# Performance work log

Hardware: AMD Instinct MI355X
Metric: run time of the kernel (lower is better)

Reference implementation:

```python
import jax, jax.numpy as jnp
import numpy as np
import math

D = 512; H = 8; L = 6; FF = 2048; S = 512; B = 32; IN = 64; OUT = 1
HD = D // H
EPS = 1e-5


def _pos_encoding(seq_len, d_model):
    position = jnp.arange(seq_len, dtype=jnp.float32)[:, None]
    div_term = jnp.exp(jnp.arange(0, d_model, 2, dtype=jnp.float32) * (-math.log(10000.0) / d_model))
    ang = position * div_term  # [S, D/2]
    pe = jnp.zeros((seq_len, d_model), dtype=jnp.float32)
    pe = pe.at[:, 0::2].set(jnp.sin(ang)).at[:, 1::2].set(jnp.cos(ang))
    return pe


def _layernorm(x, g, b):
    m = jnp.mean(x, axis=-1, keepdims=True)
    v = jnp.mean((x - m) ** 2, axis=-1, keepdims=True)
    return (x - m) * jax.lax.rsqrt(v + EPS) * g + b


def setup_inputs() -> dict:
    key = jax.random.key(0)
    ks = jax.random.split(key, 20)
    s = 0.02
    return {
        "src": jax.random.normal(ks[0], (B, S, IN), dtype=jnp.float32),
        "inp_w": jax.random.uniform(ks[1], (D, IN), minval=-0.1, maxval=0.1, dtype=jnp.float32),
        "inp_b": jnp.zeros((D,), dtype=jnp.float32),
        "in_proj_w": jax.random.normal(ks[2], (L, 3 * D, D), dtype=jnp.float32) * s,
        "in_proj_b": jnp.zeros((L, 3 * D), dtype=jnp.float32),
        "out_w": jax.random.normal(ks[3], (L, D, D), dtype=jnp.float32) * s,
        "out_b": jnp.zeros((L, D), dtype=jnp.float32),
        "ff_w1": jax.random.normal(ks[4], (L, FF, D), dtype=jnp.float32) * s,
        "ff_b1": jnp.zeros((L, FF), dtype=jnp.float32),
        "ff_w2": jax.random.normal(ks[5], (L, D, FF), dtype=jnp.float32) * s,
        "ff_b2": jnp.zeros((L, D), dtype=jnp.float32),
        "ln1_g": jnp.ones((L, D), dtype=jnp.float32),
        "ln1_b": jnp.zeros((L, D), dtype=jnp.float32),
        "ln2_g": jnp.ones((L, D), dtype=jnp.float32),
        "ln2_b": jnp.zeros((L, D), dtype=jnp.float32),
        "op_w1": jax.random.normal(ks[6], (FF, D), dtype=jnp.float32) * s,
        "op_b1": jnp.zeros((FF,), dtype=jnp.float32),
        "op_w2": jax.random.normal(ks[7], (OUT, FF), dtype=jnp.float32) * s,
        "op_b2": jnp.zeros((OUT,), dtype=jnp.float32),
    }


def reference(src, inp_w, inp_b, in_proj_w, in_proj_b, out_w, out_b,
              ff_w1, ff_b1, ff_w2, ff_b2, ln1_g, ln1_b, ln2_g, ln2_b,
              op_w1, op_b1, op_w2, op_b2):
    # input projection + sqrt(d_model) scale + positional encoding
    x = (src @ inp_w.T + inp_b) * math.sqrt(D)
    x = x + _pos_encoding(S, D)[None, :, :]
    scale = 1.0 / math.sqrt(HD)
    for i in range(L):
        # self-attention (torch nn.MultiheadAttention, eval mode, no mask)
        qkv = x @ in_proj_w[i].T + in_proj_b[i]            # [B,S,3D]
        q, k, v = jnp.split(qkv, 3, axis=-1)
        q = q.reshape(B, S, H, HD).transpose(0, 2, 1, 3)   # [B,H,S,HD]
        k = k.reshape(B, S, H, HD).transpose(0, 2, 1, 3)
        v = v.reshape(B, S, H, HD).transpose(0, 2, 1, 3)
        scores = jnp.einsum('bhqd,bhkd->bhqk', q, k) * scale
        attn = jax.nn.softmax(scores, axis=-1)             # [B,H,S,S]
        o = jnp.einsum('bhqk,bhkd->bhqd', attn, v)
        o = o.transpose(0, 2, 1, 3).reshape(B, S, D)
        o = o @ out_w[i].T + out_b[i]
        x = _layernorm(x + o, ln1_g[i], ln1_b[i])
        # feedforward
        h = jax.nn.relu(x @ ff_w1[i].T + ff_b1[i])
        ff = h @ ff_w2[i].T + ff_b2[i]
        x = _layernorm(x + ff, ln2_g[i], ln2_b[i])
    # take last timestep, output projection MLP
    last = x[:, -1, :]                                     # [B,D]
    h = jax.nn.relu(last @ op_w1.T + op_b1)
    return h @ op_w2.T + op_b2                             # [B,OUT]
```

## Files before the change

kernel.cpp:

```cpp
#include <hip/hip_runtime.h>

typedef short s16x8 __attribute__((ext_vector_type(8)));
typedef float f32x4 __attribute__((ext_vector_type(4)));
typedef float f32x16 __attribute__((ext_vector_type(16)));

__device__ short g_wbuf[18874368];
__device__ short g_srcb[1048576];
__device__ short g_inpwb[32768];
__device__ float g_pe[262144];
__device__ float g_hpart[256];

__device__ inline float b2f(short s) {
  union { unsigned int u; float f; } v;
  v.u = ((unsigned int)(unsigned short)s) << 16;
  return v.f;
}
__device__ inline short f2b(float f) {
  union { float f; unsigned int u; } v; v.f = f;
  unsigned int r = (v.u + 0x7fffu + ((v.u >> 16) & 1u)) >> 16;
  return (short)r;
}
__device__ inline s16x8 pack8(float4 a, float4 b) {
  s16x8 r;
  r[0] = f2b(a.x); r[1] = f2b(a.y); r[2] = f2b(a.z); r[3] = f2b(a.w);
  r[4] = f2b(b.x); r[5] = f2b(b.y); r[6] = f2b(b.z); r[7] = f2b(b.w);
  return r;
}

__device__ inline f32x4 mfma16(s16x8 a, s16x8 b, f32x4 c) {
  return __builtin_amdgcn_mfma_f32_16x16x32_bf16(a, b, c, 0, 0, 0);
}
__device__ inline f32x16 mfma32(s16x8 a, s16x8 b, f32x16 c) {
  return __builtin_amdgcn_mfma_f32_32x32x16_bf16(a, b, c, 0, 0, 0);
}

typedef const __attribute__((address_space(1))) void* as1cptr;
typedef __attribute__((address_space(3))) void* as3ptr;
__device__ inline void gl2lds16(const short* g, short* l) {
  __builtin_amdgcn_global_load_lds((as1cptr)g, (as3ptr)l, 16, 0, 0);
}

__global__ void __launch_bounds__(256)
cvt2_kernel(const float* __restrict__ i0, const float* __restrict__ i1) {
  const int b = blockIdx.x;
  const float* src; short* dst; int base;
  if (b < 512) { src = i0; dst = g_srcb; base = b; }
  else         { src = i1; dst = g_inpwb; base = b - 512; }
  const int idx = (base * 256 + threadIdx.x) * 8;
  float4 a = *(const float4*)(src + idx);
  float4 c = *(const float4*)(src + idx + 4);
  *(s16x8*)(dst + idx) = pack8(a, c);
}

__global__ void __launch_bounds__(256)
cvt6_kernel(const float* __restrict__ i0, const float* __restrict__ i1,
            const float* __restrict__ i2, const float* __restrict__ i3) {
  const int b = blockIdx.x;
  const float* src; short* dst; int base;
  if (b < 2304)      { src = i0; dst = g_wbuf;            base = b; }
  else if (b < 3072) { src = i1; dst = g_wbuf +  4718592; base = b - 2304; }
  else if (b < 6144) { src = i2; dst = g_wbuf +  6291456; base = b - 3072; }
  else               { src = i3; dst = g_wbuf + 12582912; base = b - 6144; }
  const int idx = (base * 256 + threadIdx.x) * 8;
  float4 a = *(const float4*)(src + idx);
  float4 c = *(const float4*)(src + idx + 4);
  *(s16x8*)(dst + idx) = pack8(a, c);
}

__global__ void __launch_bounds__(256)
pe_kernel() {
  const int s = blockIdx.x;
  const int n0 = threadIdx.x * 2;
  const float ang = (float)s * expf((float)n0 * -0.0179889460390160f);
  g_pe[s * 512 + n0]     = sinf(ang);
  g_pe[s * 512 + n0 + 1] = cosf(ang);
}

template <int EPI>
__global__ void __launch_bounds__(256, 3)
gemm_bt(const short* __restrict__ Ain, int woff, const float* __restrict__ bias,
        short* __restrict__ C, int M, int N, int K) {
  __shared__ short As[128 * 64];
  __shared__ short Bs[128 * 64];
  const int tid  = threadIdx.x;
  const int lane = tid & 63;
  const int wave = tid >> 6;
  const int wr = (wave >> 1) << 6;
  const int wc = (wave & 1) << 6;
  const int l31 = lane & 31;
  const int half = lane >> 5;
  const int bm = blockIdx.x & 127;
  const int bn = blockIdx.x >> 7;

  const short* A = (EPI == 2) ? (const short*)g_srcb : Ain;
  const short* W = (EPI == 2) ? (const short*)g_inpwb : (const short*)(g_wbuf + woff);

  int srow[4], soff[4];
#pragma unroll
  for (int i = 0; i < 4; ++i) {
    const int u = i * 256 + tid;
    srow[i] = u >> 3;
    soff[i] = ((u & 7) ^ ((u >> 3) & 7)) << 3;
  }
  const int rsw = lane & 7;
  f32x16 acc[2][2] = {};

  for (int k0 = 0; k0 < K; k0 += 64) {
#pragma unroll
    for (int i = 0; i < 4; ++i) {
      gl2lds16(A + (size_t)(bm * 128 + srow[i]) * K + k0 + soff[i],
               As + (i * 256 + tid) * 8);
      gl2lds16(W + (size_t)(bn * 128 + srow[i]) * K + k0 + soff[i],
               Bs + (i * 256 + tid) * 8);
    }
    __syncthreads();
#pragma unroll
    for (int ks = 0; ks < 4; ++ks) {
      const int rchunk = ((ks * 2 + half) ^ rsw) * 8;
      s16x8 af[2], bfr[2];
#pragma unroll
      for (int i = 0; i < 2; ++i)
        af[i] = *(const s16x8*)(As + (wr + i * 32 + l31) * 64 + rchunk);
#pragma unroll
      for (int j = 0; j < 2; ++j)
        bfr[j] = *(const s16x8*)(Bs + (wc + j * 32 + l31) * 64 + rchunk);
#pragma unroll
      for (int i = 0; i < 2; ++i)
#pragma unroll
        for (int j = 0; j < 2; ++j)
          acc[i][j] = mfma32(af[i], bfr[j], acc[i][j]);
    }
    __syncthreads();
  }

#pragma unroll
  for (int j = 0; j < 2; ++j) {
    const int col = bn * 128 + wc + j * 32 + l31;
    const float bv = bias[col];
#pragma unroll
    for (int i = 0; i < 2; ++i) {
      const int rbase = bm * 128 + wr + i * 32 + half * 4;
#pragma unroll
      for (int r = 0; r < 16; ++r) {
        const int row = rbase + (r & 3) + 8 * (r >> 2);
        float v = acc[i][j][r] + bv;
        if (EPI == 1) v = fmaxf(v, 0.0f);
        if (EPI == 2) {
          const int s = row & 511;
          v = (acc[i][j][r] + bv) * 22.62741699796952f + g_pe[s * 512 + col];
        }
        C[(size_t)row * N + col] = f2b(v);
      }
    }
  }
}

__global__ void __launch_bounds__(512, 4)
attn_kernel(const short* __restrict__ qkv, short* __restrict__ ctx) {
  __shared__ short KT[64 * 72];
  __shared__ short VT[64 * 72];
  __shared__ short Pt[64 * 72];
  __shared__ float rcomb[2][4][16];
  const int tid = threadIdx.x;
  const int lane = tid & 63, wave = tid >> 6;
  const int ml = lane & 15, quad = lane >> 4;
  const int mt = wave >> 1, nh = wave & 1;
  const int qt = (blockIdx.x >> 3) & 7;
  const int bh = (blockIdx.x & 7) | ((blockIdx.x >> 6) << 3);
  const int b = bh >> 3, h = bh & 7;
  const size_t basebs = (size_t)b * 512 * 1536;
  const int hoff = h * 64;

  s16x8 qf0, qf1;
  {
    const int qrow = qt * 64 + mt * 16 + ml;
    const short* qp = qkv + basebs + (size_t)qrow * 1536 + hoff;
    qf0 = *(const s16x8*)(qp + quad * 8);
    qf1 = *(const s16x8*)(qp + 32 + quad * 8);
  }

  f32x4 sc[8][2];
#pragma unroll
  for (int rr = 0; rr < 8; ++rr) {
    {
      const int key = tid >> 3;
      const int d8 = (tid & 7) << 3;
      const short* kp = qkv + basebs + (size_t)(rr * 64 + key) * 1536 + 512 + hoff + d8;
      *(s16x8*)(KT + key * 72 + d8) = *(const s16x8*)kp;
    }
    __syncthreads();
#pragma unroll
    for (int nt = 0; nt < 2; ++nt) {
      const int nrow = nh * 32 + nt * 16 + ml;
      f32x4 sacc = {};
      s16x8 kf0 = *(const s16x8*)(KT + nrow * 72 + quad * 8);
      s16x8 kf1 = *(const s16x8*)(KT + nrow * 72 + 32 + quad * 8);
      sacc = mfma16(qf0, kf0, sacc);
      sacc = mfma16(qf1, kf1, sacc);
      sc[rr][nt] = sacc;
    }
    __syncthreads();
  }

  f32x4 rmx = sc[0][0];
#pragma unroll
  for (int rr = 0; rr < 8; ++rr)
#pragma unroll
    for (int nt = 0; nt < 2; ++nt)
#pragma unroll
      for (int r = 0; r < 4; ++r)
        rmx[r] = fmaxf(rmx[r], sc[rr][nt][r]);
#pragma unroll
  for (int off = 1; off <= 8; off <<= 1)
#pragma unroll
    for (int r = 0; r < 4; ++r)
      rmx[r] = fmaxf(rmx[r], __shfl_xor(rmx[r], off));
  if (ml == 0) {
#pragma unroll
    for (int r = 0; r < 4; ++r)
      rcomb[nh][mt][quad * 4 + r] = rmx[r];
  }
  __syncthreads();
  float rm[4];
#pragma unroll
  for (int r = 0; r < 4; ++r)
    rm[r] = 0.125f * fmaxf(rcomb[0][mt][quad * 4 + r], rcomb[1][mt][quad * 4 + r]);

  f32x4 oacc[2] = {};
  float psum[4] = {0.f, 0.f, 0.f, 0.f};
#pragma unroll
  for (int rr = 0; rr < 8; ++rr) {
#pragma unroll
    for (int nt = 0; nt < 2; ++nt) {
#pragma unroll
      for (int r = 0; r < 4; ++r) {
        float p = __expf(sc[rr][nt][r] * 0.125f - rm[r]);
        short pb = f2b(p);
        psum[r] += b2f(pb);
        Pt[(mt * 16 + quad * 4 + r) * 72 + nh * 32 + nt * 16 + ml] = pb;
      }
    }
#pragma unroll
    for (int i = 0; i < 2; ++i) {
      const int u = i * 512 + tid;
      const int kp = u >> 5;
      const int dp = u & 31;
      const short* vp = qkv + basebs + (size_t)(rr * 64 + kp * 2) * 1536 + 1024 + hoff + dp * 2;
      unsigned int u0 = *(const unsigned int*)vp;
      unsigned int u1 = *(const unsigned int*)(vp + 1536);
      *(unsigned int*)(VT + (dp * 2) * 72 + kp * 2) = (u0 & 0xffffu) | (u1 << 16);
      *(unsigned int*)(VT + (dp * 2 + 1) * 72 + kp * 2) = (u0 >> 16) | (u1 & 0xffff0000u);
    }
    __syncthreads();
#pragma unroll
    for (int ks = 0; ks < 2; ++ks) {
      s16x8 pf = *(const s16x8*)(Pt + (mt * 16 + ml) * 72 + ks * 32 + quad * 8);
#pragma unroll
      for (int n2 = 0; n2 < 2; ++n2) {
        const int nd = (nh * 2 + n2) * 16 + ml;
        s16x8 vf = *(const s16x8*)(VT + nd * 72 + ks * 32 + quad * 8);
        oacc[n2] = mfma16(pf, vf, oacc[n2]);
      }
    }
    __syncthreads();
  }

#pragma unroll
  for (int off = 1; off <= 8; off <<= 1)
#pragma unroll
    for (int r = 0; r < 4; ++r)
      psum[r] += __shfl_xor(psum[r], off);
  if (ml == 0) {
#pragma unroll
    for (int r = 0; r < 4; ++r)
      rcomb[nh][mt][quad * 4 + r] = psum[r];
  }
  __syncthreads();

#pragma unroll
  for (int r = 0; r < 4; ++r) {
    const float l = rcomb[0][mt][quad * 4 + r] + rcomb[1][mt][quad * 4 + r];
    const float rl = 1.0f / l;
    const int grow = qt * 64 + mt * 16 + quad * 4 + r;
#pragma unroll
    for (int n2 = 0; n2 < 2; ++n2) {
      const int d = (nh * 2 + n2) * 16 + ml;
      ctx[((size_t)b * 512 + grow) * 512 + hoff + d] = f2b(oacc[n2][r] * rl);
    }
  }
}

__global__ void __launch_bounds__(256)
ln_kernel(short* __restrict__ x, const short* __restrict__ o,
          const float* __restrict__ g, const float* __restrict__ bta) {
  const int row = blockIdx.x * 4 + (threadIdx.x >> 6);
  const int lane = threadIdx.x & 63;
  short* xp = x + (size_t)row * 512 + lane * 8;
  const short* op = o + (size_t)row * 512 + lane * 8;
  s16x8 xv = *(const s16x8*)xp;
  s16x8 ov = *(const s16x8*)op;
  float v[8]; float s = 0.f, s2 = 0.f;
#pragma unroll
  for (int e = 0; e < 8; ++e) {
    float f = b2f(xv[e]) + b2f(ov[e]);
    v[e] = f; s += f; s2 += f * f;
  }
#pragma unroll
  for (int off = 32; off >= 1; off >>= 1) {
    s += __shfl_xor(s, off);
    s2 += __shfl_xor(s2, off);
  }
  const float mean = s * (1.f / 512.f);
  const float var = s2 * (1.f / 512.f) - mean * mean;
  const float rstd = rsqrtf(var + 1e-5f);
  float4 g0 = *(const float4*)(g + lane * 8);
  float4 g1 = *(const float4*)(g + lane * 8 + 4);
  float4 b0 = *(const float4*)(bta + lane * 8);
  float4 b1 = *(const float4*)(bta + lane * 8 + 4);
  float gv[8] = {g0.x, g0.y, g0.z, g0.w, g1.x, g1.y, g1.z, g1.w};
  float bv[8] = {b0.x, b0.y, b0.z, b0.w, b1.x, b1.y, b1.z, b1.w};
  s16x8 outv;
#pragma unroll
  for (int e = 0; e < 8; ++e)
    outv[e] = f2b((v[e] - mean) * rstd * gv[e] + bv[e]);
  *(s16x8*)xp = outv;
}

__global__ void __launch_bounds__(256)
head1_kernel(const short* __restrict__ x, const float* __restrict__ w1,
             const float* __restrict__ b1, const float* __restrict__ w2) {
  const int bidx = blockIdx.x;
  const int b = bidx >> 3, seg = bidx & 7;
  const int tid = threadIdx.x;
  __shared__ float xl[512];
  __shared__ float red[256];
  for (int n = tid; n < 512; n += 256)
    xl[n] = b2f(x[((size_t)b * 512 + 511) * 512 + n]);
  __syncthreads();
  const int f = seg * 256 + tid;
  const float* wr = w1 + (size_t)f * 512;
  float hv = 0.f;
  for (int k8 = 0; k8 < 64; ++k8) {
    float4 wa = *(const float4*)(wr + k8 * 8);
    float4 wb = *(const float4*)(wr + k8 * 8 + 4);
    hv += xl[k8 * 8 + 0] * wa.x + xl[k8 * 8 + 1] * wa.y +
          xl[k8 * 8 + 2] * wa.z + xl[k8 * 8 + 3] * wa.w +
          xl[k8 * 8 + 4] * wb.x + xl[k8 * 8 + 5] * wb.y +
          xl[k8 * 8 + 6] * wb.z + xl[k8 * 8 + 7] * wb.w;
  }
  hv += b1[f];
  hv = fmaxf(hv, 0.f);
  red[tid] = hv * w2[f];
  __syncthreads();
  for (int stride = 128; stride > 0; stride >>= 1) {
    if (tid < stride) red[tid] += red[tid + stride];
    __syncthreads();
  }
  if (tid == 0) g_hpart[bidx] = red[0];
}

__global__ void __launch_bounds__(64)
head2_kernel(const float* __restrict__ b2, float* __restrict__ out) {
  const int t = threadIdx.x;
  if (t < 32) {
    float s = 0.f;
#pragma unroll
    for (int c = 0; c < 8; ++c) s += g_hpart[t * 8 + c];
    out[t] = s + b2[0];
  }
}

extern "C" void kernel_launch(void* const* d_in, const int* in_sizes, int n_in,
                              void* d_out, int out_size, void* d_ws, size_t ws_size,
                              hipStream_t stream) {
  (void)in_sizes; (void)n_in; (void)out_size; (void)ws_size;
  const float* src       = (const float*)d_in[0];
  const float* inp_w     = (const float*)d_in[1];
  const float* inp_b     = (const float*)d_in[2];
  const float* in_proj_w = (const float*)d_in[3];
  const float* in_proj_b = (const float*)d_in[4];
  const float* out_w     = (const float*)d_in[5];
  const float* out_b     = (const float*)d_in[6];
  const float* ff_w1     = (const float*)d_in[7];
  const float* ff_b1     = (const float*)d_in[8];
  const float* ff_w2     = (const float*)d_in[9];
  const float* ff_b2     = (const float*)d_in[10];
  const float* ln1_g     = (const float*)d_in[11];
  const float* ln1_b     = (const float*)d_in[12];
  const float* ln2_g     = (const float*)d_in[13];
  const float* ln2_b     = (const float*)d_in[14];
  const float* op_w1     = (const float*)d_in[15];
  const float* op_b1     = (const float*)d_in[16];
  const float* op_w2     = (const float*)d_in[17];
  const float* op_b2     = (const float*)d_in[18];

  short* ws   = (short*)d_ws;
  short* x    = ws;
  short* qkv  = ws + 8388608;
  short* ctx  = qkv + 25165824;
  short* obuf = ctx + 8388608;
  short* h    = qkv;

  cvt2_kernel<<<528, 256, 0, stream>>>(src, inp_w);
  cvt6_kernel<<<9216, 256, 0, stream>>>(in_proj_w, out_w, ff_w1, ff_w2);
  pe_kernel<<<512, 256, 0, stream>>>();
  gemm_bt<2><<<512, 256, 0, stream>>>(nullptr, 0, inp_b, x, 16384, 512, 64);

  for (int l = 0; l < 6; ++l) {
    const int w_qkv = l * 786432;
    const int w_out = 4718592 + l * 262144;
    const int w_ff1 = 6291456 + l * 1048576;
    const int w_ff2 = 12582912 + l * 1048576;
    gemm_bt<0><<<1536, 256, 0, stream>>>(
        x, w_qkv, in_proj_b + l * 1536, qkv, 16384, 1536, 512);
    attn_kernel<<<2048, 512, 0, stream>>>(qkv, ctx);
    gemm_bt<0><<<512, 256, 0, stream>>>(
        ctx, w_out, out_b + l * 512, obuf, 16384, 512, 512);
    ln_kernel<<<4096, 256, 0, stream>>>(x, obuf, ln1_g + l * 512, ln1_b + l * 512);
    gemm_bt<1><<<2048, 256, 0, stream>>>(
        x, w_ff1, ff_b1 + l * 2048, h, 16384, 2048, 512);
    gemm_bt<0><<<512, 256, 0, stream>>>(
        h, w_ff2, ff_b2 + l * 512, obuf, 16384, 512, 2048);
    ln_kernel<<<4096, 256, 0, stream>>>(x, obuf, ln2_g + l * 512, ln2_b + l * 512);
  }
  head1_kernel<<<256, 256, 0, stream>>>(x, op_w1, op_b1, op_w2);
  head2_kernel<<<1, 64, 0, stream>>>(op_b2, (float*)d_out);
}
```

Before: 1.545 ms.

## Double-buffer K/V tiles with async LDS loads and XOR-swizzled layouts in attention

The attention kernel now processes keys in 128-wide tiles instead of 64. K tiles are double-buffered in shared memory via direct global-to-LDS loads, and V is prefetched into registers so the next tile loads while the current one computes. Padded LDS rows are replaced by XOR-swizzled layouts to avoid bank conflicts, and V is transposed from 16-byte loads. This halves the number of barriers and hides load latency, at the cost of more shared memory and registers, which may reduce occupancy.

```diff
diff --git a/kernel.cpp b/kernel.cpp
--- a/kernel.cpp
+++ b/kernel.cpp
@@ -157,9 +157,8 @@
 
 __global__ void __launch_bounds__(512, 4)
 attn_kernel(const short* __restrict__ qkv, short* __restrict__ ctx) {
-  __shared__ short KT[64 * 72];
-  __shared__ short VT[64 * 72];
-  __shared__ short Pt[64 * 72];
+  __shared__ short KV[2][8192];
+  __shared__ short Pt[8192];
   __shared__ float rcomb[2][4][16];
   const int tid = threadIdx.x;
   const int lane = tid & 63, wave = tid >> 6;
@@ -179,87 +178,125 @@
     qf1 = *(const s16x8*)(qp + 32 + quad * 8);
   }
 
-  f32x4 sc[8][2];
-#pragma unroll
-  for (int rr = 0; rr < 8; ++rr) {
-    {
-      const int key = tid >> 3;
-      const int d8 = (tid & 7) << 3;
-      const short* kp = qkv + basebs + (size_t)(rr * 64 + key) * 1536 + 512 + hoff + d8;
-      *(s16x8*)(KT + key * 72 + d8) = *(const s16x8*)kp;
-    }
-    __syncthreads();
-#pragma unroll
-    for (int nt = 0; nt < 2; ++nt) {
-      const int nrow = nh * 32 + nt * 16 + ml;
-      f32x4 sacc = {};
-      s16x8 kf0 = *(const s16x8*)(KT + nrow * 72 + quad * 8);
-      s16x8 kf1 = *(const s16x8*)(KT + nrow * 72 + 32 + quad * 8);
-      sacc = mfma16(qf0, kf0, sacc);
-      sacc = mfma16(qf1, kf1, sacc);
-      sc[rr][nt] = sacc;
-    }
-    __syncthreads();
-  }
-
-  f32x4 rmx = sc[0][0];
-#pragma unroll
-  for (int rr = 0; rr < 8; ++rr)
-#pragma unroll
-    for (int nt = 0; nt < 2; ++nt)
+  const int srow0 = tid >> 3, srow1 = srow0 + 64;
+  const int soff0 = (((tid & 7) ^ (srow0 & 7)) << 3);
+  const int soff1 = (((tid & 7) ^ (srow1 & 7)) << 3);
+  const short* kbase = qkv + basebs + 512 + hoff;
+
+  const int vkp = tid & 63, vd8 = (tid >> 6) << 3;
+  const short* vbase = qkv + basebs + 1024 + hoff + vd8;
+  s16x8 va, vb;
+
+  gl2lds16(kbase + (size_t)srow0 * 1536 + soff0, &KV[0][tid * 8]);
+  gl2lds16(kbase + (size_t)srow1 * 1536 + soff1, &KV[0][(512 + tid) * 8]);
+  __syncthreads();
+
+  f32x4 sc[4][4];
+#pragma unroll
+  for (int rr = 0; rr < 4; ++rr) {
+    if (rr < 3) {
+      const short* kb = kbase + (size_t)((rr + 1) * 128) * 1536;
+      short* dst = &KV[(rr + 1) & 1][0];
+      gl2lds16(kb + (size_t)srow0 * 1536 + soff0, dst + tid * 8);
+      gl2lds16(kb + (size_t)srow1 * 1536 + soff1, dst + (512 + tid) * 8);
+    } else {
+      const short* vp = vbase + (size_t)(vkp * 2) * 1536;
+      va = *(const s16x8*)vp;
+      vb = *(const s16x8*)(vp + 1536);
+    }
+    const short* kbuf = &KV[rr & 1][0];
+#pragma unroll
+    for (int nt = 0; nt < 4; ++nt) {
+      const int krow = nh * 64 + nt * 16 + ml;
+      const short* kr = kbuf + krow * 64;
+      s16x8 kf0 = *(const s16x8*)(kr + ((quad ^ (ml & 7)) << 3));
+      s16x8 kf1 = *(const s16x8*)(kr + (((quad + 4) ^ (ml & 7)) << 3));
+      f32x4 s0 = {};
+      s0 = mfma16(qf0, kf0, s0);
+      s0 = mfma16(qf1, kf1, s0);
+      sc[rr][nt] = s0;
+    }
+    if (rr == 3) {
+      short* vt = &KV[0][0];
+#pragma unroll
+      for (int j = 0; j < 8; ++j) {
+        const int d = vd8 + j;
+        unsigned int u = (unsigned int)(unsigned short)va[j]
+                       | ((unsigned int)(unsigned short)vb[j] << 16);
+        *(unsigned int*)(vt + d * 128 + ((((vkp >> 2) ^ (d & 15)) << 3) | ((vkp & 3) << 1))) = u;
+      }
+    }
+    __syncthreads();
+  }
+
+  float rm[4];
+  {
+    f32x4 rmx = sc[0][0];
+#pragma unroll
+    for (int rr = 0; rr < 4; ++rr)
+#pragma unroll
+      for (int nt = 0; nt < 4; ++nt)
+#pragma unroll
+        for (int r = 0; r < 4; ++r)
+          rmx[r] = fmaxf(rmx[r], sc[rr][nt][r]);
+#pragma unroll
+    for (int off = 1; off <= 8; off <<= 1)
 #pragma unroll
       for (int r = 0; r < 4; ++r)
-        rmx[r] = fmaxf(rmx[r], sc[rr][nt][r]);
-#pragma unroll
-  for (int off = 1; off <= 8; off <<= 1)
+        rmx[r] = fmaxf(rmx[r], __shfl_xor(rmx[r], off));
+    if (ml == 0) {
+#pragma unroll
+      for (int r = 0; r < 4; ++r)
+        rcomb[nh][mt][quad * 4 + r] = rmx[r];
+    }
+    __syncthreads();
 #pragma unroll
     for (int r = 0; r < 4; ++r)
-      rmx[r] = fmaxf(rmx[r], __shfl_xor(rmx[r], off));
-  if (ml == 0) {
-#pragma unroll
-    for (int r = 0; r < 4; ++r)
-      rcomb[nh][mt][quad * 4 + r] = rmx[r];
-  }
-  __syncthreads();
-  float rm[4];
-#pragma unroll
-  for (int r = 0; r < 4; ++r)
-    rm[r] = 0.125f * fmaxf(rcomb[0][mt][quad * 4 + r], rcomb[1][mt][quad * 4 + r]);
+      rm[r] = 0.125f * fmaxf(rcomb[0][mt][quad * 4 + r], rcomb[1][mt][quad * 4 + r]);
+  }
 
   f32x4 oacc[2] = {};
   float psum[4] = {0.f, 0.f, 0.f, 0.f};
 #pragma unroll
-  for (int rr = 0; rr < 8; ++rr) {
-#pragma unroll
-    for (int nt = 0; nt < 2; ++nt) {
+  for (int rr = 0; rr < 4; ++rr) {
+    if (rr < 3) {
+      const short* vp = vbase + (size_t)((rr + 1) * 128 + vkp * 2) * 1536;
+      va = *(const s16x8*)vp;
+      vb = *(const s16x8*)(vp + 1536);
+    }
+#pragma unroll
+    for (int nt = 0; nt < 4; ++nt) {
 #pragma unroll
       for (int r = 0; r < 4; ++r) {
         float p = __expf(sc[rr][nt][r] * 0.125f - rm[r]);
         short pb = f2b(p);
         psum[r] += b2f(pb);
-        Pt[(mt * 16 + quad * 4 + r) * 72 + nh * 32 + nt * 16 + ml] = pb;
+        const int qrl = mt * 16 + quad * 4 + r;
+        const int c = nh * 64 + nt * 16 + ml;
+        Pt[qrl * 128 + ((((c >> 3) ^ (qrl & 15)) << 3) | (c & 7))] = pb;
       }
     }
-#pragma unroll
-    for (int i = 0; i < 2; ++i) {
-      const int u = i * 512 + tid;
-      const int kp = u >> 5;
-      const int dp = u & 31;
-      const short* vp = qkv + basebs + (size_t)(rr * 64 + kp * 2) * 1536 + 1024 + hoff + dp * 2;
-      unsigned int u0 = *(const unsigned int*)vp;
-      unsigned int u1 = *(const unsigned int*)(vp + 1536);
-      *(unsigned int*)(VT + (dp * 2) * 72 + kp * 2) = (u0 & 0xffffu) | (u1 << 16);
-      *(unsigned int*)(VT + (dp * 2 + 1) * 72 + kp * 2) = (u0 >> 16) | (u1 & 0xffff0000u);
-    }
-    __syncthreads();
-#pragma unroll
-    for (int ks = 0; ks < 2; ++ks) {
-      s16x8 pf = *(const s16x8*)(Pt + (mt * 16 + ml) * 72 + ks * 32 + quad * 8);
+    __syncthreads();
+    const short* vbuf = &KV[rr & 1][0];
+    const int prow = mt * 16 + ml;
+#pragma unroll
+    for (int ks = 0; ks < 4; ++ks) {
+      s16x8 pf = *(const s16x8*)(Pt + prow * 128 + ((((ks << 2) | quad) ^ ml) << 3));
 #pragma unroll
       for (int n2 = 0; n2 < 2; ++n2) {
         const int nd = (nh * 2 + n2) * 16 + ml;
-        s16x8 vf = *(const s16x8*)(VT + nd * 72 + ks * 32 + quad * 8);
+        s16x8 vf = *(const s16x8*)(vbuf + nd * 128 + ((((ks << 2) | quad) ^ ml) << 3));
         oacc[n2] = mfma16(pf, vf, oacc[n2]);
+      }
+    }
+    if (rr < 3) {
+      short* vt = &KV[(rr + 1) & 1][0];
+#pragma unroll
+      for (int j = 0; j < 8; ++j) {
+        const int d = vd8 + j;
+        unsigned int u = (unsigned int)(unsigned short)va[j]
+                       | ((unsigned int)(unsigned short)vb[j] << 16);
+        *(unsigned int*)(vt + d * 128 + ((((vkp >> 2) ^ (d & 15)) << 3) | ((vkp & 3) << 1))) = u;
       }
     }
     __syncthreads();
```

Result: no change. 1.524 ms (-1.4%).
